# Performance work log

Measured on AMD Instinct MI355X. Metric: run time of the kernel, lower is better.

Reference implementation:

```python
import jax, jax.numpy as jnp
import numpy as np
from jax import lax

IOU_THRESHOLD = 0.1
B, N = 4, 8192


def setup_inputs() -> dict:
    key = jax.random.key(0)
    # [B, 5, N]: rows 0..3 = cx, cy, w, h; row 4 = confidence score in (0, 1)
    outputs = jax.random.uniform(key, (B, 5, N), dtype=jnp.float32)
    return {"outputs": outputs}


def _nms_single(p):
    """Greedy NMS on one image. p: [5, N] -> [5, N] with kept boxes
    compacted to the front (original column order preserved) and the rest
    zero-padded. Matches the torch loop: repeatedly take the highest-scoring
    surviving box, drop all boxes with IoU >= threshold (box keeps itself),
    and drop boxes with score <= 0."""
    boxes, scores = p[:4], p[4]
    n = scores.shape[0]
    order = jnp.argsort(-scores)            # descending score order
    b = boxes[:, order]

    x1 = b[0] - b[2] * 0.5
    y1 = b[1] - b[3] * 0.5
    x2 = b[0] + b[2] * 0.5
    y2 = b[1] + b[3] * 0.5
    area = (x2 - x1) * (y2 - y1)

    iw = jnp.clip(jnp.minimum(x2[:, None], x2[None, :]) - jnp.maximum(x1[:, None], x1[None, :]), 0.0)
    ih = jnp.clip(jnp.minimum(y2[:, None], y2[None, :]) - jnp.maximum(y1[:, None], y1[None, :]), 0.0)
    inter = iw * ih
    union = area[:, None] + area[None, :] - inter
    iou = inter / (union + 1e-8)            # [N, N] in sorted order

    idx_range = jnp.arange(n)
    keep_init = scores[order] > 0           # non_zero_scores filter

    def body(i, keep):
        # if box i (in score order) survives, suppress j with IoU >= thr, j != i
        row_keep = (iou[i] < IOU_THRESHOLD) | (idx_range == i)
        return jnp.where(keep[i], keep & row_keep, keep)

    keep_sorted = lax.fori_loop(0, n, body, keep_init)

    # map keep mask back to original column order
    keep_orig = jnp.zeros((n,), bool).at[order].set(keep_sorted)
    # stable compaction: kept columns first, original relative order preserved
    perm = jnp.argsort(jnp.where(keep_orig, 0, 1), stable=True)
    gathered = p[:, perm]                    # [5, N]
    valid = idx_range < jnp.sum(keep_orig)
    return jnp.where(valid[None, :], gathered, 0.0)


def reference(outputs):
    # torch version pads to the max detections across the batch; here we keep
    # the fixed width N (extra columns are zero), same kept values/order.
    return jax.vmap(_nms_single)(outputs)


if __name__ == "__main__":
    inp = setup_inputs()
    out = jax.jit(reference)(**inp)
    print(out.shape, out.dtype)
```

## Files before the change

### kernel.cpp

```cpp
#include <hip/hip_runtime.h>

#pragma clang fp contract(off)

#define NBOX 8192
#define BLK  1024
#define NBUCK 2048
#define IOU_THR 0.1f

typedef unsigned int u32;
typedef unsigned long long u64;

__global__ __launch_bounds__(BLK) void nms_kernel(const float* __restrict__ in,
                                                  float* __restrict__ out) {
    const int img = blockIdx.x;
    const float* __restrict__ p = in + (size_t)img * 5 * NBOX;
    float* __restrict__ o = out + (size_t)img * 5 * NBOX;
    const int t = threadIdx.x;
    const int lane = t & 63;
    const int wid = t >> 6;

    __shared__ u64 skey[NBOX];
    __shared__ u32 hist[NBUCK];
    __shared__ u32 bbase[NBUCK];
    __shared__ u32 bcur[NBUCK];
    __shared__ u32 kom[NBOX / 32];
    __shared__ u32 pfx[NBOX / 32];
    __shared__ float kx1[64], ky1[64], kx2[64], ky2[64], kar[64];
    __shared__ int wsum[BLK / 64];
    __shared__ int S0_sh, nk_sh;

    for (int i = t; i < NBUCK; i += BLK) hist[i] = 0;
    for (int i = t; i < NBOX / 32; i += BLK) kom[i] = 0;
    if (t == 0) S0_sh = 0;
    __syncthreads();

    u32 mybucket[8];
    for (int e = 0; e < 8; e++) {
        int j = t + e * BLK;
        float s = p[4 * NBOX + j];
        int vb = (int)(s * (float)NBUCK);
        vb = vb < 0 ? 0 : (vb > NBUCK - 1 ? NBUCK - 1 : vb);
        int b = NBUCK - 1 - vb;
        mybucket[e] = (u32)b;
        atomicAdd(&hist[b], 1u);
    }
    __syncthreads();

    {
        u32 h0 = hist[2 * t], h1 = hist[2 * t + 1];
        int v = (int)(h0 + h1);
        int x = v;
        for (int d = 1; d < 64; d <<= 1) {
            int y = __shfl_up(x, d, 64);
            if (lane >= d) x += y;
        }
        if (lane == 63) wsum[wid] = x;
        __syncthreads();
        int wb = 0;
        for (int i = 0; i < wid; i++) wb += wsum[i];
        int excl = wb + x - v;
        bbase[2 * t] = (u32)excl;
        bbase[2 * t + 1] = (u32)excl + h0;
        bcur[2 * t] = (u32)excl;
        bcur[2 * t + 1] = (u32)excl + h0;
    }
    __syncthreads();

    for (int e = 0; e < 8; e++) {
        int j = t + e * BLK;
        float s = p[4 * NBOX + j];
        u32 u = __float_as_uint(s);
        u32 ordb = u ^ (u32)(((int)u >> 31) | (int)0x80000000);
        u32 inv = ~ordb;
        u32 pos = atomicAdd(&bcur[mybucket[e]], 1u);
        skey[pos] = ((u64)inv << 32) | (u32)j;
    }
    __syncthreads();

    for (int b = t; b < NBUCK; b += BLK) {
        int lo = (int)bbase[b];
        int hi = lo + (int)hist[b];
        for (int i = lo + 1; i < hi; i++) {
            u64 x = skey[i];
            int j2 = i - 1;
            while (j2 >= lo && skey[j2] > x) { skey[j2 + 1] = skey[j2]; j2--; }
            skey[j2 + 1] = x;
        }
    }
    __syncthreads();

    u32 myidx[8];
    int vcnt = 0;
    for (int e = 0; e < 8; e++) {
        u64 k = skey[t * 8 + e];
        myidx[e] = (u32)k;
        if ((u32)(k >> 32) < 0x7FFFFFFFu) vcnt++;
    }
    __syncthreads();
    u32* sidx = (u32*)skey;
    for (int e = 0; e < 8; e++) sidx[t * 8 + e] = myidx[e];
    atomicAdd(&S0_sh, vcnt);
    __syncthreads();

    int S = S0_sh;

    while (S > 0) {
        int nb = S < 64 ? S : 64;

        if (wid == 0) {
            int j = -1;
            float x1 = 0, y1 = 0, x2 = 0, y2 = 0, ar = 0;
            int alive = 0;
            if (lane < nb) {
                j = (int)sidx[lane];
                float cx = p[0 * NBOX + j], cy = p[1 * NBOX + j];
                float w = p[2 * NBOX + j], h = p[3 * NBOX + j];
                x1 = cx - w * 0.5f; y1 = cy - h * 0.5f;
                x2 = cx + w * 0.5f; y2 = cy + h * 0.5f;
                ar = (x2 - x1) * (y2 - y1);
                alive = 1;
            }
            for (int l = 0; l < nb; l++) {
                u64 m = __ballot(alive);
                if ((m >> l) & 1ull) {
                    float bx1 = __shfl(x1, l, 64), by1 = __shfl(y1, l, 64);
                    float bx2 = __shfl(x2, l, 64), by2 = __shfl(y2, l, 64);
                    float bar = __shfl(ar, l, 64);
                    if (lane > l && alive) {
                        float iw = fminf(x2, bx2) - fmaxf(x1, bx1); iw = fmaxf(iw, 0.0f);
                        float ih = fminf(y2, by2) - fmaxf(y1, by1); ih = fmaxf(ih, 0.0f);
                        float inter = iw * ih;
                        float uni = bar + ar - inter;
                        float iou = inter / (uni + 1e-8f);
                        if (iou >= IOU_THR) alive = 0;
                    }
                }
            }
            u64 m = __ballot(alive);
            if (alive) {
                int q = (int)__popcll(m & ((1ull << lane) - 1ull));
                kx1[q] = x1; ky1[q] = y1; kx2[q] = x2; ky2[q] = y2; kar[q] = ar;
                atomicOr(&kom[j >> 5], 1u << (j & 31));
            }
            if (lane == 0) nk_sh = (int)__popcll(m);
        }
        __syncthreads();

        int nk = nk_sh;
        int tail = S - nb;
        int C = (tail + BLK - 1) / BLK;
        u32 sv[8];
        int mloc = 0;
        int st = nb + t * C;
        int en = st + C; if (en > S) en = S;
        for (int pos2 = st; pos2 < en; pos2++) {
            int j = (int)sidx[pos2];
            float cx = p[0 * NBOX + j], cy = p[1 * NBOX + j];
            float w = p[2 * NBOX + j], h = p[3 * NBOX + j];
            float x1 = cx - w * 0.5f, y1 = cy - h * 0.5f;
            float x2 = cx + w * 0.5f, y2 = cy + h * 0.5f;
            float ar = (x2 - x1) * (y2 - y1);
            bool ok = true;
            for (int c = 0; c < nk; c++) {
                float iw = fminf(x2, kx2[c]) - fmaxf(x1, kx1[c]); iw = fmaxf(iw, 0.0f);
                float ih = fminf(y2, ky2[c]) - fmaxf(y1, ky1[c]); ih = fmaxf(ih, 0.0f);
                float inter = iw * ih;
                float uni = kar[c] + ar - inter;
                float iou = inter / (uni + 1e-8f);
                if (iou >= IOU_THR) { ok = false; break; }
            }
            if (ok) sv[mloc++] = (u32)j;
        }
        {
            int x = mloc;
            for (int d = 1; d < 64; d <<= 1) {
                int y = __shfl_up(x, d, 64);
                if (lane >= d) x += y;
            }
            if (lane == 63) wsum[wid] = x;
            __syncthreads();
            int wb = 0, tot = 0;
            for (int i = 0; i < BLK / 64; i++) {
                int v = wsum[i];
                if (i < wid) wb += v;
                tot += v;
            }
            int off = wb + x - mloc;
            for (int q = 0; q < mloc; q++) sidx[off + q] = sv[q];
            __syncthreads();
            S = tot;
        }
    }

    if (t == 0) {
        u32 run = 0;
        for (int i = 0; i < NBOX / 32; i++) { pfx[i] = run; run += (u32)__popc(kom[i]); }
    }
    __syncthreads();
    float4 z4; z4.x = z4.y = z4.z = z4.w = 0.0f;
    float4* o4 = (float4*)o;
    for (int i = t; i < 5 * NBOX / 4; i += BLK) o4[i] = z4;
    __syncthreads();
    for (int j = t; j < NBOX; j += BLK) {
        u32 km = kom[j >> 5];
        if ((km >> (j & 31)) & 1u) {
            int pos2 = (int)(pfx[j >> 5] + (u32)__popc(km & ((1u << (j & 31)) - 1u)));
            for (int r = 0; r < 5; r++) o[r * NBOX + pos2] = p[r * NBOX + j];
        }
    }
}

extern "C" void kernel_launch(void* const* d_in, const int* in_sizes, int n_in,
                              void* d_out, int out_size, void* d_ws, size_t ws_size,
                              hipStream_t stream) {
    const float* in = (const float*)d_in[0];
    float* out = (float*)d_out;
    int B = in_sizes[0] / (5 * NBOX);
    hipLaunchKernelGGL(nms_kernel, dim3(B), dim3(BLK), 0, stream, in, out);
}
```

Before: 175.3 us.

## Keep surviving boxes in registers and replace bucket insertion sort with rank-by-count

Replaces the per-bucket serial insertion sort with a parallel rank computation: each element counts the smaller keys in its bucket. Each thread keeps the coordinates of its 8 score-ordered boxes in registers with an alive bitmask, so the shared-memory compaction and global reloads each round go away. The 64-box leader batch is resolved with ballot-based greedy suppression and then applied to the register-resident boxes. Output zeroing moves to a separate kernel, and the kept-mask prefix becomes a parallel scan. In exchange, every thread re-tests all its live boxes against each kept box every round, and the extra kernel launch adds overhead.

```diff
diff --git a/kernel.cpp b/kernel.cpp
--- a/kernel.cpp
+++ b/kernel.cpp
@@ -4,11 +4,17 @@
 
 #define NBOX 8192
 #define BLK  1024
+#define EPT  8
 #define NBUCK 2048
 #define IOU_THR 0.1f
 
 typedef unsigned int u32;
 typedef unsigned long long u64;
+
+__global__ void zero_kernel(float4* __restrict__ o, int n4) {
+    int i = blockIdx.x * blockDim.x + threadIdx.x;
+    if (i < n4) { float4 z; z.x = z.y = z.z = z.w = 0.0f; o[i] = z; }
+}
 
 __global__ __launch_bounds__(BLK) void nms_kernel(const float* __restrict__ in,
                                                   float* __restrict__ out) {
@@ -20,29 +26,30 @@
     const int wid = t >> 6;
 
     __shared__ u64 skey[NBOX];
+    __shared__ u32 sidx[NBOX];
     __shared__ u32 hist[NBUCK];
     __shared__ u32 bbase[NBUCK];
-    __shared__ u32 bcur[NBUCK];
     __shared__ u32 kom[NBOX / 32];
     __shared__ u32 pfx[NBOX / 32];
-    __shared__ float kx1[64], ky1[64], kx2[64], ky2[64], kar[64];
-    __shared__ int wsum[BLK / 64];
-    __shared__ int S0_sh, nk_sh;
+    __shared__ float4 bx4[64];
+    __shared__ int wcnt[BLK / 64];
 
     for (int i = t; i < NBUCK; i += BLK) hist[i] = 0;
     for (int i = t; i < NBOX / 32; i += BLK) kom[i] = 0;
-    if (t == 0) S0_sh = 0;
-    __syncthreads();
-
-    u32 mybucket[8];
-    for (int e = 0; e < 8; e++) {
+    __syncthreads();
+
+    u32 mybkt[EPT], myarr[EPT], mykeyhi[EPT];
+#pragma unroll
+    for (int e = 0; e < EPT; e++) {
         int j = t + e * BLK;
         float s = p[4 * NBOX + j];
+        u32 u = __float_as_uint(s);
+        u32 ordb = u ^ (u32)(((int)u >> 31) | (int)0x80000000);
+        mykeyhi[e] = ~ordb;
         int vb = (int)(s * (float)NBUCK);
         vb = vb < 0 ? 0 : (vb > NBUCK - 1 ? NBUCK - 1 : vb);
-        int b = NBUCK - 1 - vb;
-        mybucket[e] = (u32)b;
-        atomicAdd(&hist[b], 1u);
+        mybkt[e] = (u32)(NBUCK - 1 - vb);
+        myarr[e] = atomicAdd(&hist[mybkt[e]], 1u);
     }
     __syncthreads();
 
@@ -54,158 +61,156 @@
             int y = __shfl_up(x, d, 64);
             if (lane >= d) x += y;
         }
-        if (lane == 63) wsum[wid] = x;
+        if (lane == 63) wcnt[wid] = x;
         __syncthreads();
         int wb = 0;
-        for (int i = 0; i < wid; i++) wb += wsum[i];
+        for (int i = 0; i < wid; i++) wb += wcnt[i];
         int excl = wb + x - v;
         bbase[2 * t] = (u32)excl;
         bbase[2 * t + 1] = (u32)excl + h0;
-        bcur[2 * t] = (u32)excl;
-        bcur[2 * t + 1] = (u32)excl + h0;
-    }
-    __syncthreads();
-
-    for (int e = 0; e < 8; e++) {
-        int j = t + e * BLK;
+    }
+    __syncthreads();
+
+#pragma unroll
+    for (int e = 0; e < EPT; e++) {
+        u32 pos = bbase[mybkt[e]] + myarr[e];
+        skey[pos] = ((u64)mykeyhi[e] << 32) | (u32)(t + e * BLK);
+    }
+    __syncthreads();
+
+#pragma unroll
+    for (int e = 0; e < EPT; e++) {
+        u32 b = mybkt[e];
+        u32 lo = bbase[b], hi2 = lo + hist[b];
+        u64 me = ((u64)mykeyhi[e] << 32) | (u32)(t + e * BLK);
+        u32 r = lo;
+        for (u32 q = lo; q < hi2; q++) r += (skey[q] < me) ? 1u : 0u;
+        sidx[r] = (u32)me;
+    }
+    __syncthreads();
+
+    float X1[EPT], Y1[EPT], X2[EPT], Y2[EPT];
+    int OI[EPT];
+    u32 amask = 0;
+#pragma unroll
+    for (int e = 0; e < EPT; e++) {
+        int j = (int)sidx[t * EPT + e];
+        OI[e] = j;
+        float cx = p[j], cy = p[NBOX + j];
+        float w = p[2 * NBOX + j], h = p[3 * NBOX + j];
         float s = p[4 * NBOX + j];
-        u32 u = __float_as_uint(s);
-        u32 ordb = u ^ (u32)(((int)u >> 31) | (int)0x80000000);
-        u32 inv = ~ordb;
-        u32 pos = atomicAdd(&bcur[mybucket[e]], 1u);
-        skey[pos] = ((u64)inv << 32) | (u32)j;
-    }
-    __syncthreads();
-
-    for (int b = t; b < NBUCK; b += BLK) {
-        int lo = (int)bbase[b];
-        int hi = lo + (int)hist[b];
-        for (int i = lo + 1; i < hi; i++) {
-            u64 x = skey[i];
-            int j2 = i - 1;
-            while (j2 >= lo && skey[j2] > x) { skey[j2 + 1] = skey[j2]; j2--; }
-            skey[j2 + 1] = x;
-        }
-    }
-    __syncthreads();
-
-    u32 myidx[8];
-    int vcnt = 0;
-    for (int e = 0; e < 8; e++) {
-        u64 k = skey[t * 8 + e];
-        myidx[e] = (u32)k;
-        if ((u32)(k >> 32) < 0x7FFFFFFFu) vcnt++;
-    }
-    __syncthreads();
-    u32* sidx = (u32*)skey;
-    for (int e = 0; e < 8; e++) sidx[t * 8 + e] = myidx[e];
-    atomicAdd(&S0_sh, vcnt);
-    __syncthreads();
-
-    int S = S0_sh;
-
-    while (S > 0) {
+        X1[e] = cx - w * 0.5f; Y1[e] = cy - h * 0.5f;
+        X2[e] = cx + w * 0.5f; Y2[e] = cy + h * 0.5f;
+        if (s > 0.0f) amask |= (1u << e);
+    }
+
+    while (true) {
+        int myAlive = __popc(amask);
+        int x = myAlive;
+        for (int d = 1; d < 64; d <<= 1) {
+            int y = __shfl_up(x, d, 64);
+            if (lane >= d) x += y;
+        }
+        if (lane == 63) wcnt[wid] = x;
+        __syncthreads();
+        int wb = 0, S = 0;
+        for (int i = 0; i < BLK / 64; i++) {
+            int v = wcnt[i];
+            if (i < wid) wb += v;
+            S += v;
+        }
+        if (S == 0) break;
         int nb = S < 64 ? S : 64;
-
-        if (wid == 0) {
-            int j = -1;
-            float x1 = 0, y1 = 0, x2 = 0, y2 = 0, ar = 0;
-            int alive = 0;
-            if (lane < nb) {
-                j = (int)sidx[lane];
-                float cx = p[0 * NBOX + j], cy = p[1 * NBOX + j];
-                float w = p[2 * NBOX + j], h = p[3 * NBOX + j];
-                x1 = cx - w * 0.5f; y1 = cy - h * 0.5f;
-                x2 = cx + w * 0.5f; y2 = cy + h * 0.5f;
-                ar = (x2 - x1) * (y2 - y1);
-                alive = 1;
+        int r = wb + x - myAlive;
+
+        u64 slotpk = 0;
+#pragma unroll
+        for (int e = 0; e < EPT; e++) {
+            if (amask & (1u << e)) {
+                if (r < 64) {
+                    bx4[r] = make_float4(X1[e], Y1[e], X2[e], Y2[e]);
+                    slotpk |= ((u64)(u32)(r + 1)) << (8 * e);
+                }
+                r++;
             }
-            for (int l = 0; l < nb; l++) {
-                u64 m = __ballot(alive);
-                if ((m >> l) & 1ull) {
-                    float bx1 = __shfl(x1, l, 64), by1 = __shfl(y1, l, 64);
-                    float bx2 = __shfl(x2, l, 64), by2 = __shfl(y2, l, 64);
-                    float bar = __shfl(ar, l, 64);
-                    if (lane > l && alive) {
-                        float iw = fminf(x2, bx2) - fmaxf(x1, bx1); iw = fmaxf(iw, 0.0f);
-                        float ih = fminf(y2, by2) - fmaxf(y1, by1); ih = fmaxf(ih, 0.0f);
-                        float inter = iw * ih;
-                        float uni = bar + ar - inter;
-                        float iou = inter / (uni + 1e-8f);
-                        if (iou >= IOU_THR) alive = 0;
-                    }
+        }
+        __syncthreads();
+
+        float4 bb = bx4[lane < nb ? lane : 0];
+        float barL = (bb.z - bb.x) * (bb.w - bb.y);
+        u64 aliveb = (nb >= 64) ? ~0ull : ((1ull << nb) - 1ull);
+        u64 kept = 0;
+        while (aliveb) {
+            int l = __builtin_ctzll(aliveb);
+            kept |= (1ull << l);
+            aliveb &= ~(1ull << l);
+            float4 cb = bx4[l];
+            float car = (cb.z - cb.x) * (cb.w - cb.y);
+            float iw = fminf(bb.z, cb.z) - fmaxf(bb.x, cb.x); iw = fmaxf(iw, 0.0f);
+            float ih = fminf(bb.w, cb.w) - fmaxf(bb.y, cb.y); ih = fmaxf(ih, 0.0f);
+            float inter = iw * ih;
+            float uni = car + barL - inter;
+            bool sup = (lane < nb) && (lane != l) && (inter / (uni + 1e-8f) >= IOU_THR);
+            u64 sm = __ballot(sup);
+            aliveb &= ~sm;
+        }
+
+#pragma unroll
+        for (int e = 0; e < EPT; e++) {
+            int se = (int)((slotpk >> (8 * e)) & 0xFFull);
+            if (se) {
+                se--;
+                if ((kept >> se) & 1ull) atomicOr(&kom[OI[e] >> 5], 1u << (OI[e] & 31));
+                amask &= ~(1u << e);
+            }
+        }
+
+        u64 k2 = kept;
+        while (k2 && amask) {
+            int c = __builtin_ctzll(k2);
+            k2 &= k2 - 1;
+            float4 cb = bx4[c];
+            float car = (cb.z - cb.x) * (cb.w - cb.y);
+#pragma unroll
+            for (int e = 0; e < EPT; e++) {
+                if (amask & (1u << e)) {
+                    float iw = fminf(X2[e], cb.z) - fmaxf(X1[e], cb.x); iw = fmaxf(iw, 0.0f);
+                    float ih = fminf(Y2[e], cb.w) - fmaxf(Y1[e], cb.y); ih = fmaxf(ih, 0.0f);
+                    float inter = iw * ih;
+                    float arE = (X2[e] - X1[e]) * (Y2[e] - Y1[e]);
+                    float uni = car + arE - inter;
+                    if (inter / (uni + 1e-8f) >= IOU_THR) amask &= ~(1u << e);
                 }
             }
-            u64 m = __ballot(alive);
-            if (alive) {
-                int q = (int)__popcll(m & ((1ull << lane) - 1ull));
-                kx1[q] = x1; ky1[q] = y1; kx2[q] = x2; ky2[q] = y2; kar[q] = ar;
-                atomicOr(&kom[j >> 5], 1u << (j & 31));
-            }
-            if (lane == 0) nk_sh = (int)__popcll(m);
-        }
-        __syncthreads();
-
-        int nk = nk_sh;
-        int tail = S - nb;
-        int C = (tail + BLK - 1) / BLK;
-        u32 sv[8];
-        int mloc = 0;
-        int st = nb + t * C;
-        int en = st + C; if (en > S) en = S;
-        for (int pos2 = st; pos2 < en; pos2++) {
-            int j = (int)sidx[pos2];
-            float cx = p[0 * NBOX + j], cy = p[1 * NBOX + j];
-            float w = p[2 * NBOX + j], h = p[3 * NBOX + j];
-            float x1 = cx - w * 0.5f, y1 = cy - h * 0.5f;
-            float x2 = cx + w * 0.5f, y2 = cy + h * 0.5f;
-            float ar = (x2 - x1) * (y2 - y1);
-            bool ok = true;
-            for (int c = 0; c < nk; c++) {
-                float iw = fminf(x2, kx2[c]) - fmaxf(x1, kx1[c]); iw = fmaxf(iw, 0.0f);
-                float ih = fminf(y2, ky2[c]) - fmaxf(y1, ky1[c]); ih = fmaxf(ih, 0.0f);
-                float inter = iw * ih;
-                float uni = kar[c] + ar - inter;
-                float iou = inter / (uni + 1e-8f);
-                if (iou >= IOU_THR) { ok = false; break; }
-            }
-            if (ok) sv[mloc++] = (u32)j;
-        }
-        {
-            int x = mloc;
-            for (int d = 1; d < 64; d <<= 1) {
-                int y = __shfl_up(x, d, 64);
-                if (lane >= d) x += y;
-            }
-            if (lane == 63) wsum[wid] = x;
-            __syncthreads();
-            int wb = 0, tot = 0;
-            for (int i = 0; i < BLK / 64; i++) {
-                int v = wsum[i];
-                if (i < wid) wb += v;
-                tot += v;
-            }
-            int off = wb + x - mloc;
-            for (int q = 0; q < mloc; q++) sidx[off + q] = sv[q];
-            __syncthreads();
-            S = tot;
-        }
-    }
-
-    if (t == 0) {
-        u32 run = 0;
-        for (int i = 0; i < NBOX / 32; i++) { pfx[i] = run; run += (u32)__popc(kom[i]); }
-    }
-    __syncthreads();
-    float4 z4; z4.x = z4.y = z4.z = z4.w = 0.0f;
-    float4* o4 = (float4*)o;
-    for (int i = t; i < 5 * NBOX / 4; i += BLK) o4[i] = z4;
-    __syncthreads();
+        }
+    }
+    __syncthreads();
+
+    {
+        u32 w = (t < NBOX / 32) ? kom[t] : 0u;
+        int c = __popc(w);
+        int x = c;
+        for (int d = 1; d < 64; d <<= 1) {
+            int y = __shfl_up(x, d, 64);
+            if (lane >= d) x += y;
+        }
+        if (lane == 63) wcnt[wid] = x;
+        __syncthreads();
+        int wb = 0;
+        for (int i = 0; i < wid; i++) wb += wcnt[i];
+        if (t < NBOX / 32) pfx[t] = (u32)(wb + x - c);
+    }
+    __syncthreads();
+
     for (int j = t; j < NBOX; j += BLK) {
         u32 km = kom[j >> 5];
         if ((km >> (j & 31)) & 1u) {
-            int pos2 = (int)(pfx[j >> 5] + (u32)__popc(km & ((1u << (j & 31)) - 1u)));
-            for (int r = 0; r < 5; r++) o[r * NBOX + pos2] = p[r * NBOX + j];
+            int pos = (int)(pfx[j >> 5] + (u32)__popc(km & ((1u << (j & 31)) - 1u)));
+            o[0 * NBOX + pos] = p[0 * NBOX + j];
+            o[1 * NBOX + pos] = p[1 * NBOX + j];
+            o[2 * NBOX + pos] = p[2 * NBOX + j];
+            o[3 * NBOX + pos] = p[3 * NBOX + j];
+            o[4 * NBOX + pos] = p[4 * NBOX + j];
         }
     }
 }
@@ -216,5 +221,8 @@
     const float* in = (const float*)d_in[0];
     float* out = (float*)d_out;
     int B = in_sizes[0] / (5 * NBOX);
+    int n4 = B * 5 * NBOX / 4;
+    hipLaunchKernelGGL(zero_kernel, dim3((n4 + 255) / 256), dim3(256), 0, stream,
+                       (float4*)out, n4);
     hipLaunchKernelGGL(nms_kernel, dim3(B), dim3(BLK), 0, stream, in, out);
 }
```

Result: slower. 548.6 us (+213.0%).
